# Kernel tuning notes

Hardware: AMD Instinct MI355X
Metric: run time of the kernel (lower is better)

Reference implementation:

```python
import jax, jax.numpy as jnp
import numpy as np

N_NODES = 50000
N_EDGES = 800000
HID = 96

def setup_inputs() -> dict:
    key = jax.random.key(0)
    ks = jax.random.split(key, 12)
    s = 1.0 / np.sqrt(HID)
    return {
        "x_feat": jax.random.normal(ks[0], (N_NODES, HID), jnp.float32),
        "bases": jax.random.normal(ks[1], (N_EDGES, HID), jnp.float32) * 0.1,
        "W_pre": jax.random.normal(ks[2], (HID, HID), jnp.float32) * s,
        "b_pre": jax.random.normal(ks[3], (HID,), jnp.float32) * s,
        "W1": jax.random.normal(ks[4], (HID, HID), jnp.float32) * s,
        "b1": jax.random.normal(ks[5], (HID,), jnp.float32) * s,
        "W2": jax.random.normal(ks[6], (HID, HID), jnp.float32) * s,
        "b2": jax.random.normal(ks[7], (HID,), jnp.float32) * s,
        "src": jax.random.randint(ks[8], (N_EDGES,), 0, N_NODES, jnp.int32),
        "dst": jax.random.randint(ks[9], (N_EDGES,), 0, N_NODES, jnp.int32),
    }

def _gelu(x):
    return jax.nn.gelu(x, approximate=False)  # torch nn.GELU default = erf

def reference(x_feat, bases, W_pre, b_pre, W1, b1, W2, b2, src, dst):
    n = x_feat.shape[0]
    # pre_ffn: Linear + GELU on node features
    h = _gelu(x_feat @ W_pre + b_pre)                      # [N, H]
    # update_all(u_mul_e('x','v'), sum): gather src feats, weight by edge bases, scatter-add to dst
    msg = h[src] * bases                                   # [E, H]
    aggr = jax.ops.segment_sum(msg, dst, num_segments=n)   # [N, H]
    # dropout is identity in eval mode (rate=0)
    x = x_feat + aggr                                      # residual 1
    y = _gelu(_gelu(x @ W1 + b1) @ W2 + b2)                # ffn (no batch norm)
    return x + y                                           # residual 2
```

## Files before the change

### kernel.cpp

```cpp
#include <hip/hip_runtime.h>

#define NODES 50000
#define EDGES 800000
#define H 96
#define CAP 64

typedef float floatx4 __attribute__((ext_vector_type(4)));
typedef unsigned short ushort8 __attribute__((ext_vector_type(8)));
typedef __bf16 bf16x8 __attribute__((ext_vector_type(8)));

static __device__ __forceinline__ unsigned short f2b(float f) {
    unsigned int u = __float_as_uint(f);
    u = u + 0x7fffu + ((u >> 16) & 1u);
    return (unsigned short)(u >> 16);
}
static __device__ __forceinline__ float b2f(unsigned short u) {
    return __uint_as_float(((unsigned int)u) << 16);
}
static __device__ __forceinline__ float gelu_erf(float x) {
    return 0.5f * x * (1.0f + erff(x * 0.70710678118654752f));
}
static __device__ __forceinline__ bf16x8 pack_bf8(const float* a) {
    union { ushort8 u; bf16x8 v; } r;
    #pragma unroll
    for (int j = 0; j < 8; ++j) r.u[j] = f2b(a[j]);
    return r.v;
}

__global__ __launch_bounds__(256) void pre_scatter(
    const float* __restrict__ A,
    const float* __restrict__ W,
    const float* __restrict__ bias,
    unsigned short* __restrict__ outp,
    const int* __restrict__ dst,
    const int* __restrict__ src,
    int* __restrict__ count,
    int2* __restrict__ csr,
    int nStrips, int nGemmBlocks)
{
    __shared__ unsigned short Wt[96][104];
    const int tid = threadIdx.x;

    if (blockIdx.x >= nGemmBlocks) {
        const int e = (blockIdx.x - nGemmBlocks) * 256 + tid;
        if (e < EDGES) {
            const int d = dst[e];
            const int c = atomicAdd(&count[d], 1);
            if (c < CAP) {
                int2 es; es.x = e; es.y = src[e];
                csr[d * CAP + c] = es;
            }
        }
        return;
    }

    #pragma unroll
    for (int j = 0; j < 36; ++j) {
        const int f = tid + 256 * j;
        const int k = f / 96, n = f - k * 96;
        Wt[n][k] = f2b(W[f]);
    }
    __syncthreads();

    const int lane = tid & 63;
    const int quad = lane >> 4;
    const int l16  = lane & 15;

    bf16x8 Bf[3][6];
    float  bv[6];
    #pragma unroll
    for (int ks = 0; ks < 3; ++ks)
        #pragma unroll
        for (int nt = 0; nt < 6; ++nt)
            Bf[ks][nt] = *(const bf16x8*)(&Wt[nt * 16 + l16][ks * 32 + quad * 8]);
    #pragma unroll
    for (int nt = 0; nt < 6; ++nt) bv[nt] = bias[nt * 16 + l16];

    const int gwave  = (blockIdx.x * 256 + tid) >> 6;
    const int nWaves = (nGemmBlocks * 256) >> 6;

    for (int strip = gwave; strip < nStrips; strip += nWaves) {
        const int row0 = strip * 16;
        const float* Ap = A + (size_t)(row0 + l16) * H + quad * 8;

        bf16x8 Af[3];
        #pragma unroll
        for (int ks = 0; ks < 3; ++ks) {
            float tmp[8];
            const floatx4 a0 = *(const floatx4*)(Ap + ks * 32);
            const floatx4 a1 = *(const floatx4*)(Ap + ks * 32 + 4);
            #pragma unroll
            for (int j = 0; j < 4; ++j) { tmp[j] = a0[j]; tmp[4 + j] = a1[j]; }
            Af[ks] = pack_bf8(tmp);
        }

        floatx4 acc[6];
        #pragma unroll
        for (int nt = 0; nt < 6; ++nt) acc[nt] = (floatx4){0.f, 0.f, 0.f, 0.f};
        #pragma unroll
        for (int ks = 0; ks < 3; ++ks)
            #pragma unroll
            for (int nt = 0; nt < 6; ++nt)
                acc[nt] = __builtin_amdgcn_mfma_f32_16x16x32_bf16(Af[ks], Bf[ks][nt], acc[nt], 0, 0, 0);

        #pragma unroll
        for (int nt = 0; nt < 6; ++nt) {
            const int col = nt * 16 + l16;
            #pragma unroll
            for (int r = 0; r < 4; ++r) {
                const int row = row0 + quad * 4 + r;
                outp[(size_t)row * H + col] = f2b(gelu_erf(acc[nt][r] + bv[nt]));
            }
        }
    }
}

__global__ __launch_bounds__(256, 8) void gather_nodes(
    const unsigned short* __restrict__ h,
    const float* __restrict__ bases,
    const int2* __restrict__ csr,
    const int* __restrict__ count,
    const float* __restrict__ x_feat,
    float* __restrict__ xb)
{
    const int t = blockIdx.x * 256 + threadIdx.x;
    const int n = t / 12;
    if (n >= NODES) return;
    const int seg = t - n * 12;
    const int so8 = seg * 8;
    const int i0 = n * CAP;
    const int i1 = i0 + min(count[n], CAP);

    floatx4 acc0 = (floatx4){0.f, 0.f, 0.f, 0.f};
    floatx4 acc1 = (floatx4){0.f, 0.f, 0.f, 0.f};

    int i = i0;
    for (; i + 1 < i1; i += 2) {
        const unsigned long long pa =
            __builtin_nontemporal_load((const unsigned long long*)&csr[i]);
        const unsigned long long pb =
            __builtin_nontemporal_load((const unsigned long long*)&csr[i + 1]);
        const int ea = (int)pa, sa = (int)(pa >> 32);
        const int eb = (int)pb, sb = (int)(pb >> 32);
        const float* bpa = bases + (size_t)ea * H + so8;
        const float* bpb = bases + (size_t)eb * H + so8;
        const floatx4 ba0 = __builtin_nontemporal_load((const floatx4*)(bpa));
        const floatx4 ba1 = __builtin_nontemporal_load((const floatx4*)(bpa + 4));
        const ushort8 hva = *(const ushort8*)(h + (size_t)sa * H + so8);
        const floatx4 bb0 = __builtin_nontemporal_load((const floatx4*)(bpb));
        const floatx4 bb1 = __builtin_nontemporal_load((const floatx4*)(bpb + 4));
        const ushort8 hvb = *(const ushort8*)(h + (size_t)sb * H + so8);
        #pragma unroll
        for (int j = 0; j < 4; ++j) {
            acc0[j] = fmaf(ba0[j], b2f(hva[j]),     acc0[j]);
            acc1[j] = fmaf(ba1[j], b2f(hva[4 + j]), acc1[j]);
        }
        #pragma unroll
        for (int j = 0; j < 4; ++j) {
            acc0[j] = fmaf(bb0[j], b2f(hvb[j]),     acc0[j]);
            acc1[j] = fmaf(bb1[j], b2f(hvb[4 + j]), acc1[j]);
        }
    }
    if (i < i1) {
        const unsigned long long pa =
            __builtin_nontemporal_load((const unsigned long long*)&csr[i]);
        const int ea = (int)pa, sa = (int)(pa >> 32);
        const float* bpa = bases + (size_t)ea * H + so8;
        const floatx4 ba0 = __builtin_nontemporal_load((const floatx4*)(bpa));
        const floatx4 ba1 = __builtin_nontemporal_load((const floatx4*)(bpa + 4));
        const ushort8 hva = *(const ushort8*)(h + (size_t)sa * H + so8);
        #pragma unroll
        for (int j = 0; j < 4; ++j) {
            acc0[j] = fmaf(ba0[j], b2f(hva[j]),     acc0[j]);
            acc1[j] = fmaf(ba1[j], b2f(hva[4 + j]), acc1[j]);
        }
    }

    const size_t no = (size_t)n * H + so8;
    const floatx4 x0 = __builtin_nontemporal_load((const floatx4*)(x_feat + no));
    const floatx4 x1 = __builtin_nontemporal_load((const floatx4*)(x_feat + no + 4));
    #pragma unroll
    for (int j = 0; j < 4; ++j) { acc0[j] += x0[j]; acc1[j] += x1[j]; }
    *(floatx4*)(xb + no)     = acc0;
    *(floatx4*)(xb + no + 4) = acc1;
}

__global__ __launch_bounds__(256) void ffn_dual(
    const float* __restrict__ A,
    const float* __restrict__ W1, const float* __restrict__ b1,
    const float* __restrict__ W2, const float* __restrict__ b2,
    float* __restrict__ outp,
    int nStrips)
{
    __shared__ unsigned short Wt1[96][104];
    __shared__ unsigned short Wt2[96][104];
    __shared__ unsigned short St[4][16][112];

    const int tid = threadIdx.x;
    #pragma unroll
    for (int j = 0; j < 36; ++j) {
        const int f = tid + 256 * j;
        const int k = f / 96, n = f - k * 96;
        Wt1[n][k] = f2b(W1[f]);
        Wt2[n][k] = f2b(W2[f]);
    }
    __syncthreads();

    const int lane = tid & 63;
    const int quad = lane >> 4;
    const int l16  = lane & 15;
    const int w    = tid >> 6;

    float bv1[6], bv2[6];
    #pragma unroll
    for (int nt = 0; nt < 6; ++nt) {
        bv1[nt] = b1[nt * 16 + l16];
        bv2[nt] = b2[nt * 16 + l16];
    }

    const int wsw = quad << 3;
    const int rsw = (l16 >> 2) << 3;

    const int gwave  = (blockIdx.x * 256 + tid) >> 6;
    const int nWaves = (gridDim.x * 256) >> 6;

    for (int strip = gwave; strip < nStrips; strip += nWaves) {
        const int row0 = strip * 16;
        const float* Ap = A + (size_t)(row0 + l16) * H + quad * 8;

        bf16x8 Af[3];
        #pragma unroll
        for (int ks = 0; ks < 3; ++ks) {
            float tmp[8];
            const floatx4 a0 = *(const floatx4*)(Ap + ks * 32);
            const floatx4 a1 = *(const floatx4*)(Ap + ks * 32 + 4);
            #pragma unroll
            for (int j = 0; j < 4; ++j) { tmp[j] = a0[j]; tmp[4 + j] = a1[j]; }
            Af[ks] = pack_bf8(tmp);
        }
        floatx4 facc[6];
        #pragma unroll
        for (int nt = 0; nt < 6; ++nt) facc[nt] = (floatx4){0.f, 0.f, 0.f, 0.f};
        #pragma unroll
        for (int ks = 0; ks < 3; ++ks)
            #pragma unroll
            for (int nt = 0; nt < 6; ++nt) {
                const bf16x8 Bf1 = *(const bf16x8*)(&Wt1[nt * 16 + l16][ks * 32 + quad * 8]);
                facc[nt] = __builtin_amdgcn_mfma_f32_16x16x32_bf16(Af[ks], Bf1, facc[nt], 0, 0, 0);
            }

        #pragma unroll
        for (int nt = 0; nt < 6; ++nt)
            #pragma unroll
            for (int r = 0; r < 4; ++r)
                St[w][quad * 4 + r][(nt * 16 + l16) ^ wsw] =
                    f2b(gelu_erf(facc[nt][r] + bv1[nt]));
        bf16x8 Tf[3];
        #pragma unroll
        for (int ks = 0; ks < 3; ++ks)
            Tf[ks] = *(const bf16x8*)(&St[w][l16][(ks * 32 + quad * 8) ^ rsw]);

        #pragma unroll
        for (int nt = 0; nt < 6; ++nt) facc[nt] = (floatx4){0.f, 0.f, 0.f, 0.f};
        #pragma unroll
        for (int ks = 0; ks < 3; ++ks)
            #pragma unroll
            for (int nt = 0; nt < 6; ++nt) {
                const bf16x8 Bf2 = *(const bf16x8*)(&Wt2[nt * 16 + l16][ks * 32 + quad * 8]);
                facc[nt] = __builtin_amdgcn_mfma_f32_16x16x32_bf16(Tf[ks], Bf2, facc[nt], 0, 0, 0);
            }
        #pragma unroll
        for (int nt = 0; nt < 6; ++nt) {
            const int col = nt * 16 + l16;
            #pragma unroll
            for (int r = 0; r < 4; ++r) {
                const int row = row0 + quad * 4 + r;
                const size_t o = (size_t)row * H + col;
                outp[o] = A[o] + gelu_erf(facc[nt][r] + bv2[nt]);
            }
        }
    }
}

extern "C" void kernel_launch(void* const* d_in, const int* in_sizes, int n_in,
                              void* d_out, int out_size, void* d_ws, size_t ws_size,
                              hipStream_t stream)
{
    const float* x_feat = (const float*)d_in[0];
    const float* bases  = (const float*)d_in[1];
    const float* W_pre  = (const float*)d_in[2];
    const float* b_pre  = (const float*)d_in[3];
    const float* W1     = (const float*)d_in[4];
    const float* b1     = (const float*)d_in[5];
    const float* W2     = (const float*)d_in[6];
    const float* b2     = (const float*)d_in[7];
    const int* src = (const int*)d_in[8];
    const int* dst = (const int*)d_in[9];

    char* ws = (char*)d_ws;
    int*            count  = (int*)(ws);
    int2*           csr2   = (int2*)(ws + 1048576);
    unsigned short* h_bf   = (unsigned short*)(ws + 27262976);
    float*          xb     = (float*)(ws + 37748736);
    float*          out    = (float*)d_out;

    const int nStrips     = NODES / 16;
    const int nGemmBlocks = 512;
    const int nScatBlocks = (EDGES + 255) / 256;

    hipMemsetAsync(count, 0, NODES * sizeof(int), stream);
    pre_scatter<<<nGemmBlocks + nScatBlocks, 256, 0, stream>>>(
        x_feat, W_pre, b_pre, h_bf, dst, src, count, csr2, nStrips, nGemmBlocks);
    gather_nodes<<<(NODES * 12 + 255) / 256, 256, 0, stream>>>(
        h_bf, bases, csr2, count, x_feat, xb);
    ffn_dual<<<512, 256, 0, stream>>>(xb, W1, b1, W2, b2, out, nStrips);
}
```

Measured before the change: 536.0 us.

## Vectorize edge scatter to four edges per thread and use cached CSR loads

The scatter part of pre_scatter now handles four edges per thread, loading dst and src as int4 and issuing four independent atomics before the CSR writes. This cuts the scatter grid to a quarter of the blocks. The gather kernel reads CSR entries through normal cached int2 loads instead of nontemporal loads, and its launch-bounds occupancy hint drops from 8 to 6 blocks. The aim is fewer scatter blocks with more memory-level parallelism per thread, plus better cache reuse of CSR lines, at the cost of fewer threads to hide atomic latency.

```diff
diff --git a/kernel.cpp b/kernel.cpp
--- a/kernel.cpp
+++ b/kernel.cpp
@@ -42,13 +42,34 @@
     const int tid = threadIdx.x;
 
     if (blockIdx.x >= nGemmBlocks) {
-        const int e = (blockIdx.x - nGemmBlocks) * 256 + tid;
-        if (e < EDGES) {
-            const int d = dst[e];
-            const int c = atomicAdd(&count[d], 1);
-            if (c < CAP) {
-                int2 es; es.x = e; es.y = src[e];
-                csr[d * CAP + c] = es;
+        const int base = ((blockIdx.x - nGemmBlocks) * 256 + tid) * 4;
+        if (base + 3 < EDGES) {
+            const int4 d4 = *(const int4*)(dst + base);
+            const int4 s4 = *(const int4*)(src + base);
+            const int dd[4] = {d4.x, d4.y, d4.z, d4.w};
+            const int ss[4] = {s4.x, s4.y, s4.z, s4.w};
+            int cc[4];
+            #pragma unroll
+            for (int j = 0; j < 4; ++j) cc[j] = atomicAdd(&count[dd[j]], 1);
+            #pragma unroll
+            for (int j = 0; j < 4; ++j) {
+                if (cc[j] < CAP) {
+                    int2 es; es.x = base + j; es.y = ss[j];
+                    csr[dd[j] * CAP + cc[j]] = es;
+                }
+            }
+        } else if (base < EDGES) {
+            #pragma unroll
+            for (int j = 0; j < 4; ++j) {
+                const int e = base + j;
+                if (e < EDGES) {
+                    const int d = dst[e];
+                    const int c = atomicAdd(&count[d], 1);
+                    if (c < CAP) {
+                        int2 es; es.x = e; es.y = src[e];
+                        csr[d * CAP + c] = es;
+                    }
+                }
             }
         }
         return;
@@ -115,7 +136,7 @@
     }
 }
 
-__global__ __launch_bounds__(256, 8) void gather_nodes(
+__global__ __launch_bounds__(256, 6) void gather_nodes(
     const unsigned short* __restrict__ h,
     const float* __restrict__ bases,
     const int2* __restrict__ csr,
@@ -136,20 +157,16 @@
 
     int i = i0;
     for (; i + 1 < i1; i += 2) {
-        const unsigned long long pa =
-            __builtin_nontemporal_load((const unsigned long long*)&csr[i]);
-        const unsigned long long pb =
-            __builtin_nontemporal_load((const unsigned long long*)&csr[i + 1]);
-        const int ea = (int)pa, sa = (int)(pa >> 32);
-        const int eb = (int)pb, sb = (int)(pb >> 32);
-        const float* bpa = bases + (size_t)ea * H + so8;
-        const float* bpb = bases + (size_t)eb * H + so8;
+        const int2 ea = csr[i];
+        const int2 eb = csr[i + 1];
+        const float* bpa = bases + (size_t)ea.x * H + so8;
+        const float* bpb = bases + (size_t)eb.x * H + so8;
         const floatx4 ba0 = __builtin_nontemporal_load((const floatx4*)(bpa));
         const floatx4 ba1 = __builtin_nontemporal_load((const floatx4*)(bpa + 4));
-        const ushort8 hva = *(const ushort8*)(h + (size_t)sa * H + so8);
+        const ushort8 hva = *(const ushort8*)(h + (size_t)ea.y * H + so8);
         const floatx4 bb0 = __builtin_nontemporal_load((const floatx4*)(bpb));
         const floatx4 bb1 = __builtin_nontemporal_load((const floatx4*)(bpb + 4));
-        const ushort8 hvb = *(const ushort8*)(h + (size_t)sb * H + so8);
+        const ushort8 hvb = *(const ushort8*)(h + (size_t)eb.y * H + so8);
         #pragma unroll
         for (int j = 0; j < 4; ++j) {
             acc0[j] = fmaf(ba0[j], b2f(hva[j]),     acc0[j]);
@@ -162,13 +179,11 @@
         }
     }
     if (i < i1) {
-        const unsigned long long pa =
-            __builtin_nontemporal_load((const unsigned long long*)&csr[i]);
-        const int ea = (int)pa, sa = (int)(pa >> 32);
-        const float* bpa = bases + (size_t)ea * H + so8;
+        const int2 ea = csr[i];
+        const float* bpa = bases + (size_t)ea.x * H + so8;
         const floatx4 ba0 = __builtin_nontemporal_load((const floatx4*)(bpa));
         const floatx4 ba1 = __builtin_nontemporal_load((const floatx4*)(bpa + 4));
-        const ushort8 hva = *(const ushort8*)(h + (size_t)sa * H + so8);
+        const ushort8 hva = *(const ushort8*)(h + (size_t)ea.y * H + so8);
         #pragma unroll
         for (int j = 0; j < 4; ++j) {
             acc0[j] = fmaf(ba0[j], b2f(hva[j]),     acc0[j]);
@@ -306,7 +321,7 @@
 
     const int nStrips     = NODES / 16;
     const int nGemmBlocks = 512;
-    const int nScatBlocks = (EDGES + 255) / 256;
+    const int nScatBlocks = (EDGES + 1023) / 1024;
 
     hipMemsetAsync(count, 0, NODES * sizeof(int), stream);
     pre_scatter<<<nGemmBlocks + nScatBlocks, 256, 0, stream>>>(
```

After: 519.1 us. -3.2%, faster.
